# Kernel optimization log

Measured on AMD Instinct MI355X. Metric: run time of the kernel, lower is better.

## Reference

```python
import jax, jax.numpy as jnp
import numpy as np
import math

B, N, M, D = 8, 2048, 2048, 512

def setup_inputs() -> dict:
    key = jax.random.key(0)
    ks = jax.random.split(key, 12)
    s = 1.0 / math.sqrt(D)
    return {
        "query_xyz": jax.random.normal(ks[0], (B, N, 3), jnp.float32),
        "query_feat": jax.random.normal(ks[1], (B, N, D), jnp.float32),
        "key_xyz": jax.random.normal(ks[2], (B, M, 3), jnp.float32),
        "key_feat": jax.random.normal(ks[3], (B, M, D), jnp.float32),
        "Wq": jax.random.normal(ks[4], (D, D), jnp.float32) * s,
        "bq": jnp.zeros((D,), jnp.float32),
        "Wk": jax.random.normal(ks[5], (D, D), jnp.float32) * s,
        "bk": jnp.zeros((D,), jnp.float32),
        "Wv": jax.random.normal(ks[6], (D, D), jnp.float32) * s,
        "bv": jnp.zeros((D,), jnp.float32),
        "Wo": jax.random.normal(ks[7], (D, D), jnp.float32) * s,
        "bo": jnp.zeros((D,), jnp.float32),
        "ln_g": jnp.ones((D,), jnp.float32),
        "ln_b": jnp.zeros((D,), jnp.float32),
    }

def reference(query_xyz, query_feat, key_xyz, key_feat,
              Wq, bq, Wk, bk, Wv, bv, Wo, bo, ln_g, ln_b):
    d = query_feat.shape[-1]
    # projections (torch Linear: x @ W.T + b)
    Q = jnp.einsum('bnd,ed->bne', query_feat, Wq) + bq
    K = jnp.einsum('bmd,ed->bme', key_feat, Wk) + bk
    V = jnp.einsum('bmd,ed->bme', key_feat, Wv) + bv
    scores = jnp.einsum('bnd,bmd->bnm', Q, K) / jnp.sqrt(jnp.float32(d))
    # pairwise euclidean distance via (||q||^2 + ||k||^2 - 2 q.k), avoids BxNxMx3
    qn = jnp.sum(query_xyz * query_xyz, axis=-1)  # [B,N]
    kn = jnp.sum(key_xyz * key_xyz, axis=-1)      # [B,M]
    d2 = qn[:, :, None] + kn[:, None, :] - 2.0 * jnp.einsum('bnc,bmc->bnm', query_xyz, key_xyz)
    dist = jnp.sqrt(jnp.maximum(d2, 1e-12))
    # distance bias: log(exp(-2*dist) + 1e-8)
    scores = scores + jnp.log(jnp.exp(-dist * 2.0) + 1e-8)
    attn = jax.nn.softmax(scores, axis=-1)
    # dropout is identity in eval mode
    attended = jnp.einsum('bnm,bme->bne', attn, V)
    out = jnp.einsum('bne,fe->bnf', attended, Wo) + bo
    x = query_feat + out
    # LayerNorm (eps=1e-5)
    mu = jnp.mean(x, axis=-1, keepdims=True)
    var = jnp.mean((x - mu) ** 2, axis=-1, keepdims=True)
    return (x - mu) * jax.lax.rsqrt(var + 1e-5) * ln_g + ln_b
```

## Files before the change

### kernel.cpp

```cpp
#include <hip/hip_runtime.h>

typedef __attribute__((ext_vector_type(8))) short short8;
typedef __attribute__((ext_vector_type(8))) unsigned short us8;
typedef __attribute__((ext_vector_type(4))) unsigned short us4;
typedef __attribute__((ext_vector_type(4))) float f32x4;

__device__ __forceinline__ float bf2f(unsigned short h) {
  return __uint_as_float(((unsigned int)h) << 16);
}
__device__ __forceinline__ unsigned short f2bf(float f) {
  unsigned int u = __float_as_uint(f);
  u += 0x7FFF + ((u >> 16) & 1);
  return (unsigned short)(u >> 16);
}

__device__ __forceinline__ void gload16(const void* g, void* l) {
  __builtin_amdgcn_global_load_lds(
      (const __attribute__((address_space(1))) unsigned int*)g,
      (__attribute__((address_space(3))) unsigned int*)l, 16, 0, 0);
}

#define BM 128
#define BN 128
#define BK 32

struct EpiParams {
  const float* bias;
  const float* aux0;
  const float* aux1;
  long  saux;
  float scale;
};

template<int EPI>
__global__ __launch_bounds__(256)
void gemm_bt(const unsigned short* __restrict__ A, const unsigned short* __restrict__ B,
             void* __restrict__ Cout, int Kd, int lda, int ldb, int ldc,
             long sA, long sB, long sC, EpiParams ep)
{
  __shared__ __attribute__((aligned(16))) char smem[16384];
  char* Al = smem;
  char* Bl = smem + 8192;

  const int t    = threadIdx.x;
  const int lane = t & 63;
  const int wid  = t >> 6;
  const int wr   = wid >> 1;
  const int wc   = wid & 1;
  const int tr   = lane & 15;
  const int tg   = lane >> 4;

  const int bz    = blockIdx.z;
  const int rbase = blockIdx.y * BM;
  const int cbase = blockIdx.x * BN;

  const unsigned short* Ab = A + (long)bz * sA;
  const unsigned short* Bb = B + (long)bz * sB;
  const char* Asrc = (const char*)(Ab + (long)rbase * lda);
  const char* Bsrc = (const char*)(Bb + (long)cbase * ldb);
  const long lda_b = (long)lda * 2;
  const long ldb_b = (long)ldb * 2;

  f32x4 acc[4][4] = {};

  for (int k0 = 0; k0 < Kd; k0 += BK) {
#pragma unroll
    for (int it = 0; it < 2; ++it) {
      const int boff = (it * 4 + wid) * 1024 + lane * 16;
      const int r  = boff >> 6;
      const int cb = boff & 63;
      gload16(Asrc + (long)r * lda_b + (k0 * 2 + cb), Al + (it * 4 + wid) * 1024);
      gload16(Bsrc + (long)r * ldb_b + (k0 * 2 + cb), Bl + (it * 4 + wid) * 1024);
    }
    __syncthreads();

    short8 af[4], bf[4];
#pragma unroll
    for (int m = 0; m < 4; ++m)
      af[m] = *(const short8*)(Al + ((wr * 64 + m * 16 + tr) * 32 + tg * 8) * 2);
#pragma unroll
    for (int n = 0; n < 4; ++n)
      bf[n] = *(const short8*)(Bl + ((wc * 64 + n * 16 + tr) * 32 + tg * 8) * 2);
#pragma unroll
    for (int m = 0; m < 4; ++m)
#pragma unroll
      for (int n = 0; n < 4; ++n)
        acc[m][n] = __builtin_amdgcn_mfma_f32_16x16x32_bf16(af[m], bf[n], acc[m][n], 0, 0, 0);
    __syncthreads();
  }

  if (EPI == 0) {
    unsigned short* C = (unsigned short*)Cout + (long)bz * sC;
#pragma unroll
    for (int n = 0; n < 4; ++n) {
      const int col = cbase + wc * 64 + n * 16 + tr;
      const float bv = ep.bias ? ep.bias[col] : 0.f;
#pragma unroll
      for (int m = 0; m < 4; ++m) {
#pragma unroll
        for (int i = 0; i < 4; ++i) {
          const int row = rbase + wr * 64 + m * 16 + tg * 4 + i;
          C[(long)row * ldc + col] = f2bf(acc[m][n][i] + bv);
        }
      }
    }
  } else if (EPI == 1) {
    unsigned short* C = (unsigned short*)Cout;
#pragma unroll
    for (int n = 0; n < 4; ++n) {
      const int col = cbase + wc * 64 + n * 16 + tr;
      const float bv = ep.bias ? ep.bias[col] : 0.f;
#pragma unroll
      for (int m = 0; m < 4; ++m) {
        const int row0 = rbase + wr * 64 + m * 16 + tg * 4;
        const int b  = row0 >> 11;
        const int ml = row0 & 2047;
        us4 v;
#pragma unroll
        for (int i = 0; i < 4; ++i) v[i] = f2bf(acc[m][n][i] + bv);
        *(us4*)(C + ((long)b * 512 + col) * 2048 + ml) = v;
      }
    }
  } else if (EPI == 2) {
    float* qs = (float*)smem;
    float* ks = (float*)smem + 384;
    if (t < 128) {
      const float* q = ep.aux0 + (long)bz * ep.saux + (long)(rbase + t) * 3;
      qs[t * 3] = q[0]; qs[t * 3 + 1] = q[1]; qs[t * 3 + 2] = q[2];
    } else {
      const int tt = t - 128;
      const float* k = ep.aux1 + (long)bz * ep.saux + (long)(cbase + tt) * 3;
      ks[tt * 3] = k[0]; ks[tt * 3 + 1] = k[1]; ks[tt * 3 + 2] = k[2];
    }
    __syncthreads();
    unsigned short* C = (unsigned short*)Cout + (long)bz * sC;
#pragma unroll
    for (int m = 0; m < 4; ++m) {
#pragma unroll
      for (int i = 0; i < 4; ++i) {
        const int rl = wr * 64 + m * 16 + tg * 4 + i;
        const float qx = qs[rl * 3], qy = qs[rl * 3 + 1], qz = qs[rl * 3 + 2];
#pragma unroll
        for (int n = 0; n < 4; ++n) {
          const int cl = wc * 64 + n * 16 + tr;
          const float dx = qx - ks[cl * 3];
          const float dy = qy - ks[cl * 3 + 1];
          const float dz = qz - ks[cl * 3 + 2];
          const float d2 = dx * dx + dy * dy + dz * dz;
          const float d  = sqrtf(fmaxf(d2, 1e-12f));
          const float bias = fmaxf(-2.f * d, -18.420680743952367f);
          C[(long)(rbase + rl) * ldc + (cbase + cl)] = f2bf(acc[m][n][i] * ep.scale + bias);
        }
      }
    }
  } else {
    float* C = (float*)Cout;
    const float* qf = ep.aux0;
#pragma unroll
    for (int n = 0; n < 4; ++n) {
      const int col = cbase + wc * 64 + n * 16 + tr;
      const float bv = ep.bias ? ep.bias[col] : 0.f;
#pragma unroll
      for (int m = 0; m < 4; ++m) {
#pragma unroll
        for (int i = 0; i < 4; ++i) {
          const int row = rbase + wr * 64 + m * 16 + tg * 4 + i;
          C[(long)row * 512 + col] = acc[m][n][i] + bv + qf[(long)row * 512 + col];
        }
      }
    }
  }
}

__global__ __launch_bounds__(256)
void softmax_rows(unsigned short* __restrict__ S)
{
  const int row  = blockIdx.x * 4 + (threadIdx.x >> 6);
  const int lane = threadIdx.x & 63;
  unsigned short* rp = S + (long)row * 2048;

  us8 v[4];
#pragma unroll
  for (int c = 0; c < 4; ++c) v[c] = *(const us8*)(rp + c * 512 + lane * 8);
  float f[32];
#pragma unroll
  for (int c = 0; c < 4; ++c)
#pragma unroll
    for (int j = 0; j < 8; ++j) f[c * 8 + j] = bf2f(v[c][j]);

  float mx = f[0];
#pragma unroll
  for (int i = 1; i < 32; ++i) mx = fmaxf(mx, f[i]);
#pragma unroll
  for (int off = 32; off; off >>= 1) mx = fmaxf(mx, __shfl_xor(mx, off, 64));

  float sum = 0.f;
#pragma unroll
  for (int i = 0; i < 32; ++i) { f[i] = __expf(f[i] - mx); sum += f[i]; }
#pragma unroll
  for (int off = 32; off; off >>= 1) sum += __shfl_xor(sum, off, 64);
  const float inv = 1.f / sum;

#pragma unroll
  for (int c = 0; c < 4; ++c) {
    us8 o;
#pragma unroll
    for (int j = 0; j < 8; ++j) o[j] = f2bf(f[c * 8 + j] * inv);
    *(us8*)(rp + c * 512 + lane * 8) = o;
  }
}

__global__ __launch_bounds__(256)
void ln_rows(const float* __restrict__ X, const float* __restrict__ g,
             const float* __restrict__ b, float* __restrict__ O)
{
  const int row  = blockIdx.x * 4 + (threadIdx.x >> 6);
  const int lane = threadIdx.x & 63;
  const float* xp = X + (long)row * 512;

  f32x4 v0 = *(const f32x4*)(xp + lane * 4);
  f32x4 v1 = *(const f32x4*)(xp + 256 + lane * 4);

  float s = 0.f;
#pragma unroll
  for (int j = 0; j < 4; ++j) s += v0[j] + v1[j];
#pragma unroll
  for (int off = 32; off; off >>= 1) s += __shfl_xor(s, off, 64);
  const float mu = s * (1.f / 512.f);

  float vs = 0.f;
#pragma unroll
  for (int j = 0; j < 4; ++j) {
    float d0 = v0[j] - mu, d1 = v1[j] - mu;
    vs += d0 * d0 + d1 * d1;
  }
#pragma unroll
  for (int off = 32; off; off >>= 1) vs += __shfl_xor(vs, off, 64);
  const float r = rsqrtf(vs * (1.f / 512.f) + 1e-5f);

  f32x4 g0 = *(const f32x4*)(g + lane * 4);
  f32x4 g1 = *(const f32x4*)(g + 256 + lane * 4);
  f32x4 b0 = *(const f32x4*)(b + lane * 4);
  f32x4 b1 = *(const f32x4*)(b + 256 + lane * 4);

  f32x4 o0, o1;
#pragma unroll
  for (int j = 0; j < 4; ++j) {
    o0[j] = (v0[j] - mu) * r * g0[j] + b0[j];
    o1[j] = (v1[j] - mu) * r * g1[j] + b1[j];
  }
  float* op = O + (long)row * 512;
  *(f32x4*)(op + lane * 4) = o0;
  *(f32x4*)(op + 256 + lane * 4) = o1;
}

__global__ __launch_bounds__(256)
void cvt_bf16(const float* __restrict__ src, unsigned short* __restrict__ dst, int nvec)
{
  const int i = blockIdx.x * blockDim.x + threadIdx.x;
  if (i >= nvec) return;
  const f32x4* s = (const f32x4*)src;
  f32x4 a = s[(long)i * 2];
  f32x4 c = s[(long)i * 2 + 1];
  us8 o;
#pragma unroll
  for (int j = 0; j < 4; ++j) { o[j] = f2bf(a[j]); o[4 + j] = f2bf(c[j]); }
  *(us8*)(dst + (long)i * 8) = o;
}

extern "C" void kernel_launch(void* const* d_in, const int* in_sizes, int n_in,
                              void* d_out, int out_size, void* d_ws, size_t ws_size,
                              hipStream_t stream)
{
  const float* qxyz  = (const float*)d_in[0];
  const float* qfeat = (const float*)d_in[1];
  const float* kxyz  = (const float*)d_in[2];
  const float* kfeat = (const float*)d_in[3];
  const float* Wq = (const float*)d_in[4];
  const float* bq = (const float*)d_in[5];
  const float* Wk = (const float*)d_in[6];
  const float* bk = (const float*)d_in[7];
  const float* Wv = (const float*)d_in[8];
  const float* bv = (const float*)d_in[9];
  const float* Wo = (const float*)d_in[10];
  const float* bo = (const float*)d_in[11];
  const float* lng = (const float*)d_in[12];
  const float* lnb = (const float*)d_in[13];

  const long SZ_FEAT = 16777216;
  char* ws = (char*)d_ws;
  if (ws_size < (size_t)153092096) return;

  unsigned short* XQ  = (unsigned short*)(ws);
  unsigned short* XK  = (unsigned short*)(ws + SZ_FEAT);
  unsigned short* QB  = (unsigned short*)(ws + 2 * SZ_FEAT);
  unsigned short* KB  = (unsigned short*)(ws + 3 * SZ_FEAT);
  unsigned short* VT  = (unsigned short*)(ws + 4 * SZ_FEAT);
  unsigned short* WQB = (unsigned short*)(ws + 5 * SZ_FEAT);
  unsigned short* WKB = WQB + 262144;
  unsigned short* WVB = WQB + 524288;
  unsigned short* WOB = WQB + 786432;
  unsigned short* SB  = (unsigned short*)(ws + 5 * SZ_FEAT + 2097152);
  unsigned short* ATT = QB;
  float* XRES = (float*)ws;

  cvt_bf16<<<4096, 256, 0, stream>>>(qfeat, XQ, 1048576);
  cvt_bf16<<<4096, 256, 0, stream>>>(kfeat, XK, 1048576);
  cvt_bf16<<<128, 256, 0, stream>>>(Wq, WQB, 32768);
  cvt_bf16<<<128, 256, 0, stream>>>(Wk, WKB, 32768);
  cvt_bf16<<<128, 256, 0, stream>>>(Wv, WVB, 32768);
  cvt_bf16<<<128, 256, 0, stream>>>(Wo, WOB, 32768);

  EpiParams e0{}; e0.bias = bq;
  gemm_bt<0><<<dim3(4, 128, 1), 256, 0, stream>>>(XQ, WQB, QB, 512, 512, 512, 512, 0, 0, 0, e0);
  EpiParams e1{}; e1.bias = bk;
  gemm_bt<0><<<dim3(4, 128, 1), 256, 0, stream>>>(XK, WKB, KB, 512, 512, 512, 512, 0, 0, 0, e1);
  EpiParams e2{}; e2.bias = bv;
  gemm_bt<1><<<dim3(4, 128, 1), 256, 0, stream>>>(XK, WVB, VT, 512, 512, 512, 0, 0, 0, 0, e2);

  EpiParams es{}; es.aux0 = qxyz; es.aux1 = kxyz; es.saux = 2048 * 3;
  es.scale = 0.044194173824159216f;
  gemm_bt<2><<<dim3(16, 16, 8), 256, 0, stream>>>(QB, KB, SB, 512, 512, 512, 2048,
                                                  (long)2048 * 512, (long)2048 * 512,
                                                  (long)2048 * 2048, es);

  softmax_rows<<<4096, 256, 0, stream>>>(SB);

  EpiParams ep{}; ep.bias = nullptr;
  gemm_bt<0><<<dim3(4, 16, 8), 256, 0, stream>>>(SB, VT, ATT, 2048, 2048, 2048, 512,
                                                 (long)2048 * 2048, (long)512 * 2048,
                                                 (long)2048 * 512, ep);

  EpiParams eo{}; eo.bias = bo; eo.aux0 = qfeat;
  gemm_bt<3><<<dim3(4, 128, 1), 256, 0, stream>>>(ATT, WOB, XRES, 512, 512, 512, 512, 0, 0, 0, eo);

  ln_rows<<<4096, 256, 0, stream>>>(XRES, lng, lnb, (float*)d_out);
}
```

Before: 303.4 us.

## Fuse score GEMM, distance bias, softmax and PV into flash-attention kernel

Replaces the three-step attention path with one online-softmax kernel: the score GEMM with a distance-bias epilogue, the row softmax, and the P·V GEMM. Each block keeps a 64-query tile of Q in registers and streams 64-key tiles of K and V^T through swizzled LDS. It keeps a running max and sum per row and rescales the accumulators after each tile. This removes the 64 MB bf16 score matrix that was written, read and rewritten, and shrinks the workspace. The cost is low occupancy: large LDS tiles and 512-thread blocks give a grid of only 256 blocks. There are also several barriers per key tile and only partial overlap of the next K/V loads with compute.

```diff
diff --git a/kernel.cpp b/kernel.cpp
--- a/kernel.cpp
+++ b/kernel.cpp
@@ -121,38 +121,6 @@
         *(us4*)(C + ((long)b * 512 + col) * 2048 + ml) = v;
       }
     }
-  } else if (EPI == 2) {
-    float* qs = (float*)smem;
-    float* ks = (float*)smem + 384;
-    if (t < 128) {
-      const float* q = ep.aux0 + (long)bz * ep.saux + (long)(rbase + t) * 3;
-      qs[t * 3] = q[0]; qs[t * 3 + 1] = q[1]; qs[t * 3 + 2] = q[2];
-    } else {
-      const int tt = t - 128;
-      const float* k = ep.aux1 + (long)bz * ep.saux + (long)(cbase + tt) * 3;
-      ks[tt * 3] = k[0]; ks[tt * 3 + 1] = k[1]; ks[tt * 3 + 2] = k[2];
-    }
-    __syncthreads();
-    unsigned short* C = (unsigned short*)Cout + (long)bz * sC;
-#pragma unroll
-    for (int m = 0; m < 4; ++m) {
-#pragma unroll
-      for (int i = 0; i < 4; ++i) {
-        const int rl = wr * 64 + m * 16 + tg * 4 + i;
-        const float qx = qs[rl * 3], qy = qs[rl * 3 + 1], qz = qs[rl * 3 + 2];
-#pragma unroll
-        for (int n = 0; n < 4; ++n) {
-          const int cl = wc * 64 + n * 16 + tr;
-          const float dx = qx - ks[cl * 3];
-          const float dy = qy - ks[cl * 3 + 1];
-          const float dz = qz - ks[cl * 3 + 2];
-          const float d2 = dx * dx + dy * dy + dz * dz;
-          const float d  = sqrtf(fmaxf(d2, 1e-12f));
-          const float bias = fmaxf(-2.f * d, -18.420680743952367f);
-          C[(long)(rbase + rl) * ldc + (cbase + cl)] = f2bf(acc[m][n][i] * ep.scale + bias);
-        }
-      }
-    }
   } else {
     float* C = (float*)Cout;
     const float* qf = ep.aux0;
@@ -172,41 +140,206 @@
   }
 }
 
-__global__ __launch_bounds__(256)
-void softmax_rows(unsigned short* __restrict__ S)
+__global__ __launch_bounds__(512, 2)
+void fused_attn(const unsigned short* Qg, const unsigned short* __restrict__ Kg,
+                const unsigned short* __restrict__ VTg,
+                const float* __restrict__ qxyzg, const float* __restrict__ kxyzg,
+                unsigned short* ATT)
 {
-  const int row  = blockIdx.x * 4 + (threadIdx.x >> 6);
-  const int lane = threadIdx.x & 63;
-  unsigned short* rp = S + (long)row * 2048;
-
-  us8 v[4];
-#pragma unroll
-  for (int c = 0; c < 4; ++c) v[c] = *(const us8*)(rp + c * 512 + lane * 8);
-  float f[32];
-#pragma unroll
-  for (int c = 0; c < 4; ++c)
-#pragma unroll
-    for (int j = 0; j < 8; ++j) f[c * 8 + j] = bf2f(v[c][j]);
-
-  float mx = f[0];
-#pragma unroll
-  for (int i = 1; i < 32; ++i) mx = fmaxf(mx, f[i]);
-#pragma unroll
-  for (int off = 32; off; off >>= 1) mx = fmaxf(mx, __shfl_xor(mx, off, 64));
-
-  float sum = 0.f;
-#pragma unroll
-  for (int i = 0; i < 32; ++i) { f[i] = __expf(f[i] - mx); sum += f[i]; }
-#pragma unroll
-  for (int off = 32; off; off >>= 1) sum += __shfl_xor(sum, off, 64);
-  const float inv = 1.f / sum;
-
-#pragma unroll
-  for (int c = 0; c < 4; ++c) {
-    us8 o;
-#pragma unroll
-    for (int j = 0; j < 8; ++j) o[j] = f2bf(f[c * 8 + j] * inv);
-    *(us8*)(rp + c * 512 + lane * 8) = o;
+  __shared__ __attribute__((aligned(16))) unsigned short sK[64 * 512];
+  __shared__ __attribute__((aligned(16))) unsigned short sVT[512 * 64];
+  __shared__ __attribute__((aligned(16))) unsigned short sP[64 * 64];
+  __shared__ __attribute__((aligned(16))) float sPmax[2][64];
+  __shared__ __attribute__((aligned(16))) float sPsum[2][64];
+  __shared__ __attribute__((aligned(16))) float sMnew[64];
+  __shared__ __attribute__((aligned(16))) float sScale[64];
+
+  const int b  = blockIdx.x;
+  const int q0 = blockIdx.y * 64;
+  const int tid  = threadIdx.x;
+  const int lane = tid & 63;
+  const int w    = tid >> 6;
+  const int tr   = lane & 15;
+  const int tg   = lane >> 4;
+  const int mq   = w & 3;
+  const int cg   = w >> 1 >> 1;
+
+  const float SCALE = 0.044194173824159216f;
+
+  const unsigned short* Qrow = Qg + ((long)b * 2048 + q0 + mq * 16 + tr) * 512;
+  short8 qf[16];
+#pragma unroll
+  for (int c = 0; c < 16; ++c) qf[c] = *(const short8*)(Qrow + c * 32 + tg * 8);
+
+  float qx[4], qy[4], qz[4];
+#pragma unroll
+  for (int i = 0; i < 4; ++i) {
+    const float* p = qxyzg + ((long)b * 2048 + q0 + mq * 16 + tg * 4 + i) * 3;
+    qx[i] = p[0]; qy[i] = p[1]; qz[i] = p[2];
+  }
+
+  f32x4 om[4][4] = {};
+  float m_run = -1e30f, l_run = 0.f;
+
+#pragma unroll
+  for (int j = 0; j < 8; ++j) {
+    const int r = w * 8 + j;
+    gload16(Kg + ((long)b * 2048 + r) * 512 + ((lane ^ (r & 7)) * 8), sK + r * 512);
+  }
+
+#pragma unroll 1
+  for (int t = 0; t < 32; ++t) {
+    const int kv0 = t * 64;
+    asm volatile("s_waitcnt vmcnt(0)" ::: "memory");
+    __builtin_amdgcn_s_barrier();
+    asm volatile("" ::: "memory");
+
+#pragma unroll
+    for (int j = 0; j < 8; ++j) {
+      const int eb = j * 64 + w * 8;
+      const int e  = eb + (lane >> 3);
+      const int sl = lane & 7;
+      gload16(VTg + ((long)b * 512 + e) * 2048 + kv0 + ((sl ^ (e & 7)) * 8), sVT + eb * 64);
+    }
+
+    float kx[2], ky[2], kz[2];
+#pragma unroll
+    for (int n = 0; n < 2; ++n) {
+      const float* p = kxyzg + ((long)b * 2048 + kv0 + cg * 32 + n * 16 + tr) * 3;
+      kx[n] = p[0]; ky[n] = p[1]; kz[n] = p[2];
+    }
+
+    f32x4 sa[2];
+    sa[0] = f32x4{0.f, 0.f, 0.f, 0.f};
+    sa[1] = f32x4{0.f, 0.f, 0.f, 0.f};
+#pragma unroll
+    for (int ks = 0; ks < 16; ++ks) {
+#pragma unroll
+      for (int n = 0; n < 2; ++n) {
+        const int r = cg * 32 + n * 16 + tr;
+        const short8 bfr = *(const short8*)((const char*)sK + r * 1024 +
+                             (((ks * 32 + tg * 8) * 2) ^ ((r & 7) << 4)));
+        sa[n] = __builtin_amdgcn_mfma_f32_16x16x32_bf16(qf[ks], bfr, sa[n], 0, 0, 0);
+      }
+    }
+
+    f32x4 pm;
+#pragma unroll
+    for (int i = 0; i < 4; ++i) {
+      float best = -1e30f;
+#pragma unroll
+      for (int n = 0; n < 2; ++n) {
+        const float dx = qx[i] - kx[n], dy = qy[i] - ky[n], dz = qz[i] - kz[n];
+        const float dd = sqrtf(fmaxf(dx * dx + dy * dy + dz * dz, 1e-12f));
+        const float v  = sa[n][i] * SCALE + fmaxf(-2.f * dd, -18.420680743952367f);
+        sa[n][i] = v;
+        best = fmaxf(best, v);
+      }
+      pm[i] = best;
+    }
+#pragma unroll
+    for (int off = 1; off <= 8; off <<= 1)
+#pragma unroll
+      for (int i = 0; i < 4; ++i) pm[i] = fmaxf(pm[i], __shfl_xor(pm[i], off, 64));
+    if (tr == 0) *(f32x4*)&sPmax[cg][mq * 16 + tg * 4] = pm;
+
+    asm volatile("s_waitcnt lgkmcnt(0)" ::: "memory");
+    __builtin_amdgcn_s_barrier();
+    asm volatile("" ::: "memory");
+
+    if (t + 1 < 32) {
+#pragma unroll
+      for (int j = 0; j < 8; ++j) {
+        const int r = w * 8 + j;
+        gload16(Kg + ((long)b * 2048 + kv0 + 64 + r) * 512 + ((lane ^ (r & 7)) * 8),
+                sK + r * 512);
+      }
+    }
+
+    if (w == 0) {
+      const float tm = fmaxf(sPmax[0][lane], sPmax[1][lane]);
+      const float mn = fmaxf(m_run, tm);
+      const float sc = __expf(m_run - mn);
+      m_run = mn; l_run *= sc;
+      sMnew[lane] = mn; sScale[lane] = sc;
+    }
+    asm volatile("s_waitcnt lgkmcnt(0)" ::: "memory");
+    __builtin_amdgcn_s_barrier();
+    asm volatile("" ::: "memory");
+
+    f32x4 ps = {0.f, 0.f, 0.f, 0.f};
+#pragma unroll
+    for (int i = 0; i < 4; ++i) {
+      const float mn = sMnew[mq * 16 + tg * 4 + i];
+      const int r = mq * 16 + tg * 4 + i;
+#pragma unroll
+      for (int n = 0; n < 2; ++n) {
+        const float p = __expf(sa[n][i] - mn);
+        ps[i] += p;
+        const int c = cg * 32 + n * 16 + tr;
+        *(unsigned short*)((char*)sP + r * 128 + ((c * 2) ^ ((r & 7) << 4))) = f2bf(p);
+      }
+    }
+#pragma unroll
+    for (int off = 1; off <= 8; off <<= 1)
+#pragma unroll
+      for (int i = 0; i < 4; ++i) ps[i] += __shfl_xor(ps[i], off, 64);
+    if (tr == 0) *(f32x4*)&sPsum[cg][mq * 16 + tg * 4] = ps;
+
+#pragma unroll
+    for (int mo = 0; mo < 4; ++mo) {
+      const f32x4 sc4 = *(const f32x4*)&sScale[mo * 16 + tg * 4];
+#pragma unroll
+      for (int n = 0; n < 4; ++n)
+#pragma unroll
+        for (int i = 0; i < 4; ++i) om[mo][n][i] *= sc4[i];
+    }
+
+    asm volatile("s_waitcnt lgkmcnt(0)" ::: "memory");
+    if (t + 1 < 32) asm volatile("s_waitcnt vmcnt(8)" ::: "memory");
+    else            asm volatile("s_waitcnt vmcnt(0)" ::: "memory");
+    __builtin_amdgcn_s_barrier();
+    asm volatile("" ::: "memory");
+
+    if (w == 0) l_run += sPsum[0][lane] + sPsum[1][lane];
+
+#pragma unroll
+    for (int ks2 = 0; ks2 < 2; ++ks2) {
+      short8 pa[4];
+#pragma unroll
+      for (int mo = 0; mo < 4; ++mo) {
+        const int r = mo * 16 + tr;
+        pa[mo] = *(const short8*)((const char*)sP + r * 128 +
+                   ((ks2 * 64 + tg * 16) ^ ((r & 7) << 4)));
+      }
+#pragma unroll
+      for (int n = 0; n < 4; ++n) {
+        const int e = w * 64 + n * 16 + tr;
+        const short8 vb = *(const short8*)((const char*)sVT + e * 128 +
+                            ((ks2 * 64 + tg * 16) ^ ((e & 7) << 4)));
+#pragma unroll
+        for (int mo = 0; mo < 4; ++mo)
+          om[mo][n] = __builtin_amdgcn_mfma_f32_16x16x32_bf16(pa[mo], vb, om[mo][n], 0, 0, 0);
+      }
+    }
+  }
+
+  if (w == 0) sScale[lane] = 1.f / l_run;
+  asm volatile("s_waitcnt lgkmcnt(0)" ::: "memory");
+  __builtin_amdgcn_s_barrier();
+  asm volatile("" ::: "memory");
+#pragma unroll
+  for (int mo = 0; mo < 4; ++mo) {
+    const f32x4 inv4 = *(const f32x4*)&sScale[mo * 16 + tg * 4];
+#pragma unroll
+    for (int n = 0; n < 4; ++n) {
+      const int col = w * 64 + n * 16 + tr;
+#pragma unroll
+      for (int i = 0; i < 4; ++i) {
+        const long row = (long)b * 2048 + q0 + mo * 16 + tg * 4 + i;
+        ATT[row * 512 + col] = f2bf(om[mo][n][i] * inv4[i]);
+      }
+    }
   }
 }
 
@@ -289,7 +422,7 @@
 
   const long SZ_FEAT = 16777216;
   char* ws = (char*)d_ws;
-  if (ws_size < (size_t)153092096) return;
+  if (ws_size < (size_t)85983232) return;
 
   unsigned short* XQ  = (unsigned short*)(ws);
   unsigned short* XK  = (unsigned short*)(ws + SZ_FEAT);
@@ -300,7 +433,6 @@
   unsigned short* WKB = WQB + 262144;
   unsigned short* WVB = WQB + 524288;
   unsigned short* WOB = WQB + 786432;
-  unsigned short* SB  = (unsigned short*)(ws + 5 * SZ_FEAT + 2097152);
   unsigned short* ATT = QB;
   float* XRES = (float*)ws;
 
@@ -318,18 +450,7 @@
   EpiParams e2{}; e2.bias = bv;
   gemm_bt<1><<<dim3(4, 128, 1), 256, 0, stream>>>(XK, WVB, VT, 512, 512, 512, 0, 0, 0, 0, e2);
 
-  EpiParams es{}; es.aux0 = qxyz; es.aux1 = kxyz; es.saux = 2048 * 3;
-  es.scale = 0.044194173824159216f;
-  gemm_bt<2><<<dim3(16, 16, 8), 256, 0, stream>>>(QB, KB, SB, 512, 512, 512, 2048,
-                                                  (long)2048 * 512, (long)2048 * 512,
-                                                  (long)2048 * 2048, es);
-
-  softmax_rows<<<4096, 256, 0, stream>>>(SB);
-
-  EpiParams ep{}; ep.bias = nullptr;
-  gemm_bt<0><<<dim3(4, 16, 8), 256, 0, stream>>>(SB, VT, ATT, 2048, 2048, 2048, 512,
-                                                 (long)2048 * 2048, (long)512 * 2048,
-                                                 (long)2048 * 512, ep);
+  fused_attn<<<dim3(8, 32), 512, 0, stream>>>(QB, KB, VT, qxyz, kxyz, ATT);
 
   EpiParams eo{}; eo.bias = bo; eo.aux0 = qfeat;
   gemm_bt<3><<<dim3(4, 128, 1), 256, 0, stream>>>(ATT, WOB, XRES, 512, 512, 512, 512, 0, 0, 0, eo);
```

Result: slower. 393.2 us (+29.6%).

## Add 256-row tile GEMM kernel for score and attention-value matmuls

Applied to the files above, without the earlier changes.

Introduces a new gemm_big kernel that computes 256x128 output tiles per block, with 8 MFMA row fragments per wave and a configurable wave-column count. It also maps the batch index to blockIdx.x so consecutive blocks work on different batches. The QK^T score GEMM with the distance-bias epilogue and the attention-times-V GEMM now use it, with 256 and 512 threads respectively. The larger tiles raise operand reuse per LDS load and cut the number of blocks. The cost is higher register pressure from the larger accumulators and fewer blocks to fill the GPU.

```diff
diff --git a/kernel.cpp b/kernel.cpp
--- a/kernel.cpp
+++ b/kernel.cpp
@@ -121,28 +121,127 @@
         *(us4*)(C + ((long)b * 512 + col) * 2048 + ml) = v;
       }
     }
-  } else if (EPI == 2) {
+  } else {
+    float* C = (float*)Cout;
+    const float* qf = ep.aux0;
+#pragma unroll
+    for (int n = 0; n < 4; ++n) {
+      const int col = cbase + wc * 64 + n * 16 + tr;
+      const float bv = ep.bias ? ep.bias[col] : 0.f;
+#pragma unroll
+      for (int m = 0; m < 4; ++m) {
+#pragma unroll
+        for (int i = 0; i < 4; ++i) {
+          const int row = rbase + wr * 64 + m * 16 + tg * 4 + i;
+          C[(long)row * 512 + col] = acc[m][n][i] + bv + qf[(long)row * 512 + col];
+        }
+      }
+    }
+  }
+}
+
+template<int EPI, int NWC>
+__global__ __launch_bounds__(128 * NWC, 2)
+void gemm_big(const unsigned short* __restrict__ A, const unsigned short* __restrict__ B,
+              void* __restrict__ Cout, int Kd, int lda, int ldb, int ldc,
+              long sA, long sB, long sC, int ntn, EpiParams ep)
+{
+  constexpr int T  = 128 * NWC;
+  constexpr int NF = 128 / (NWC * 16);
+  constexpr int RA = 16384 / (T * 16);
+  constexpr int RB = 8192 / (T * 16);
+
+  __shared__ __attribute__((aligned(16))) char smem[24576];
+  char* Al = smem;
+  char* Bl = smem + 16384;
+
+  const int t    = threadIdx.x;
+  const int lane = t & 63;
+  const int wid  = t >> 6;
+  const int wr   = wid / NWC;
+  const int wc   = wid % NWC;
+  const int tr   = lane & 15;
+  const int tg   = lane >> 4;
+
+  const int bz    = blockIdx.x;
+  const int rbase = (blockIdx.y / ntn) * 256;
+  const int cbase = (blockIdx.y % ntn) * 128;
+
+  const unsigned short* Ab = A + (long)bz * sA;
+  const unsigned short* Bb = B + (long)bz * sB;
+  const char* Asrc = (const char*)(Ab + (long)rbase * lda);
+  const char* Bsrc = (const char*)(Bb + (long)cbase * ldb);
+  const long lda_b = (long)lda * 2;
+  const long ldb_b = (long)ldb * 2;
+
+  f32x4 acc[8][NF] = {};
+
+  for (int k0 = 0; k0 < Kd; k0 += BK) {
+#pragma unroll
+    for (int r = 0; r < RA; ++r) {
+      const int o = (r * T + t) * 16;
+      gload16(Asrc + (long)(o >> 6) * lda_b + (k0 * 2 + (o & 63)),
+              Al + (r * T + wid * 64) * 16);
+    }
+#pragma unroll
+    for (int r = 0; r < RB; ++r) {
+      const int o = (r * T + t) * 16;
+      gload16(Bsrc + (long)(o >> 6) * ldb_b + (k0 * 2 + (o & 63)),
+              Bl + (r * T + wid * 64) * 16);
+    }
+    __syncthreads();
+
+    short8 af[8], bf[NF];
+#pragma unroll
+    for (int m = 0; m < 8; ++m)
+      af[m] = *(const short8*)(Al + ((wr * 128 + m * 16 + tr) * 32 + tg * 8) * 2);
+#pragma unroll
+    for (int n = 0; n < NF; ++n)
+      bf[n] = *(const short8*)(Bl + ((wc * (NF * 16) + n * 16 + tr) * 32 + tg * 8) * 2);
+#pragma unroll
+    for (int m = 0; m < 8; ++m)
+#pragma unroll
+      for (int n = 0; n < NF; ++n)
+        acc[m][n] = __builtin_amdgcn_mfma_f32_16x16x32_bf16(af[m], bf[n], acc[m][n], 0, 0, 0);
+    __syncthreads();
+  }
+
+  if (EPI == 0) {
+    unsigned short* C = (unsigned short*)Cout + (long)bz * sC;
+#pragma unroll
+    for (int n = 0; n < NF; ++n) {
+      const int col = cbase + wc * (NF * 16) + n * 16 + tr;
+#pragma unroll
+      for (int m = 0; m < 8; ++m) {
+#pragma unroll
+        for (int i = 0; i < 4; ++i) {
+          const int row = rbase + wr * 128 + m * 16 + tg * 4 + i;
+          C[(long)row * ldc + col] = f2bf(acc[m][n][i]);
+        }
+      }
+    }
+  } else {
     float* qs = (float*)smem;
-    float* ks = (float*)smem + 384;
-    if (t < 128) {
+    float* ks = (float*)smem + 768;
+    {
       const float* q = ep.aux0 + (long)bz * ep.saux + (long)(rbase + t) * 3;
       qs[t * 3] = q[0]; qs[t * 3 + 1] = q[1]; qs[t * 3 + 2] = q[2];
-    } else {
-      const int tt = t - 128;
-      const float* k = ep.aux1 + (long)bz * ep.saux + (long)(cbase + tt) * 3;
-      ks[tt * 3] = k[0]; ks[tt * 3 + 1] = k[1]; ks[tt * 3 + 2] = k[2];
+      if (t < 128) {
+        const float* k2 = ep.aux1 + (long)bz * ep.saux + (long)(cbase + t) * 3;
+        ks[t * 3] = k2[0]; ks[t * 3 + 1] = k2[1]; ks[t * 3 + 2] = k2[2];
+      }
     }
     __syncthreads();
     unsigned short* C = (unsigned short*)Cout + (long)bz * sC;
 #pragma unroll
-    for (int m = 0; m < 4; ++m) {
+    for (int m = 0; m < 8; ++m) {
 #pragma unroll
       for (int i = 0; i < 4; ++i) {
-        const int rl = wr * 64 + m * 16 + tg * 4 + i;
+        const int rl = wr * 128 + m * 16 + tg * 4 + i;
         const float qx = qs[rl * 3], qy = qs[rl * 3 + 1], qz = qs[rl * 3 + 2];
 #pragma unroll
-        for (int n = 0; n < 4; ++n) {
-          const int cl = wc * 64 + n * 16 + tr;
+        for (int n = 0; n < NF; ++n) {
+          const int cl = wc * (NF * 16) + n * 16 + tr;
           const float dx = qx - ks[cl * 3];
           const float dy = qy - ks[cl * 3 + 1];
           const float dz = qz - ks[cl * 3 + 2];
@@ -150,22 +249,6 @@
           const float d  = sqrtf(fmaxf(d2, 1e-12f));
           const float bias = fmaxf(-2.f * d, -18.420680743952367f);
           C[(long)(rbase + rl) * ldc + (cbase + cl)] = f2bf(acc[m][n][i] * ep.scale + bias);
-        }
-      }
-    }
-  } else {
-    float* C = (float*)Cout;
-    const float* qf = ep.aux0;
-#pragma unroll
-    for (int n = 0; n < 4; ++n) {
-      const int col = cbase + wc * 64 + n * 16 + tr;
-      const float bv = ep.bias ? ep.bias[col] : 0.f;
-#pragma unroll
-      for (int m = 0; m < 4; ++m) {
-#pragma unroll
-        for (int i = 0; i < 4; ++i) {
-          const int row = rbase + wr * 64 + m * 16 + tg * 4 + i;
-          C[(long)row * 512 + col] = acc[m][n][i] + bv + qf[(long)row * 512 + col];
         }
       }
     }
@@ -320,16 +403,16 @@
 
   EpiParams es{}; es.aux0 = qxyz; es.aux1 = kxyz; es.saux = 2048 * 3;
   es.scale = 0.044194173824159216f;
-  gemm_bt<2><<<dim3(16, 16, 8), 256, 0, stream>>>(QB, KB, SB, 512, 512, 512, 2048,
-                                                  (long)2048 * 512, (long)2048 * 512,
-                                                  (long)2048 * 2048, es);
+  gemm_big<2, 2><<<dim3(8, 128), 256, 0, stream>>>(QB, KB, SB, 512, 512, 512, 2048,
+                                                   (long)2048 * 512, (long)2048 * 512,
+                                                   (long)2048 * 2048, 16, es);
 
   softmax_rows<<<4096, 256, 0, stream>>>(SB);
 
-  EpiParams ep{}; ep.bias = nullptr;
-  gemm_bt<0><<<dim3(4, 16, 8), 256, 0, stream>>>(SB, VT, ATT, 2048, 2048, 2048, 512,
-                                                 (long)2048 * 2048, (long)512 * 2048,
-                                                 (long)2048 * 512, ep);
+  EpiParams ep{};
+  gemm_big<0, 4><<<dim3(8, 32), 512, 0, stream>>>(SB, VT, ATT, 2048, 2048, 2048, 512,
+                                                  (long)2048 * 2048, (long)512 * 2048,
+                                                  (long)2048 * 512, 4, ep);
 
   EpiParams eo{}; eo.bias = bo; eo.aux0 = qfeat;
   gemm_bt<3><<<dim3(4, 128, 1), 256, 0, stream>>>(ATT, WOB, XRES, 512, 512, 512, 512, 0, 0, 0, eo);
```

Result: faster. 279.5 us (-7.9%).
